# Kernel tuning notes

Hardware: AMD Instinct MI355X
Metric: run time of the kernel (lower is better)

The kernel has to match this reference:

```python
import jax, jax.numpy as jnp
import numpy as np

B, S, T, D = 4, 512, 512, 256


def setup_inputs() -> dict:
    key = jax.random.key(0)
    ks = jax.random.split(key, 10)
    scale = 1.0 / np.sqrt(D)
    return {
        "source": jax.random.normal(ks[0], (B, S, D), jnp.float32),
        "target": jax.random.normal(ks[1], (B, T, D), jnp.float32),
        "W_src": jax.random.uniform(ks[2], (D, D), jnp.float32, -scale, scale),
        "b_src": jax.random.uniform(ks[3], (D,), jnp.float32, -scale, scale),
        "W_tgt": jax.random.uniform(ks[4], (D, D), jnp.float32, -scale, scale),
        "b_tgt": jax.random.uniform(ks[5], (D,), jnp.float32, -scale, scale),
        "W_res": jax.random.uniform(ks[6], (D, 1), jnp.float32, -scale, scale),
        "b_res": jax.random.uniform(ks[7], (1,), jnp.float32, -scale, scale),
        "W_prob": jax.random.uniform(ks[8], (D, 2), jnp.float32, -scale, scale),
        "b_prob": jax.random.uniform(ks[9], (2,), jnp.float32, -scale, scale),
    }


def reference(source, target, W_src, b_src, W_tgt, b_tgt, W_res, b_res, W_prob, b_prob):
    # source: (B,S,D), target: (B,T,D)
    src_lin = jnp.einsum("bsd,de->bse", source, W_src) + b_src  # (B,S,D)
    tgt_lin = jnp.einsum("btd,de->bte", target, W_tgt) + b_tgt  # (B,T,D)
    # Bahdanau-style additive attention: (B,T,S,D) broadcast, tanh, D->1
    h = jnp.tanh(src_lin[:, None, :, :] + tgt_lin[:, :, None, :])  # (B,T,S,D)
    genP = jnp.einsum("btsd,d->bts", h, W_res[:, 0]) + b_res[0]     # (B,T,S)
    prob = jax.nn.softmax(jnp.einsum("btd,de->bte", target, W_prob) + b_prob, axis=-1)  # (B,T,2)
    return genP, prob
```

## Files before the change

kernel.cpp:

```cpp
#include <hip/hip_runtime.h>

#define B_ 4
#define S_ 512
#define T_ 512
#define D_ 256

#define K2F 2.8853900817779268f

__global__ __launch_bounds__(256) void lin_exp_kernel(
    const float* __restrict__ src, const float* __restrict__ tgt,
    const float* __restrict__ Wsrc, const float* __restrict__ bsrc,
    const float* __restrict__ Wtgt, const float* __restrict__ btgt,
    float* __restrict__ ya, float* __restrict__ yc)
{
    __shared__ float inT[D_ * 20];
    __shared__ float Wl[32 * D_];

    const int tid = threadIdx.x;
    const int nsrc_rows = B_ * S_;
    const int r0 = blockIdx.x * 16;
    const bool is_tgt = (r0 >= nsrc_rows);
    const float* in   = is_tgt ? tgt  : src;
    const float* W    = is_tgt ? Wtgt : Wsrc;
    const float* bias = is_tgt ? btgt : bsrc;
    float* out        = is_tgt ? yc   : ya;
    const int rbase   = is_tgt ? (r0 - nsrc_rows) : r0;

    {
        const int row = tid & 15;
        #pragma unroll
        for (int it = 0; it < 4; it++) {
            int kslot = it * 16 + (tid >> 4);
            int k4 = kslot * 4;
            float4 v = *(const float4*)&in[(rbase + row) * D_ + k4];
            inT[(k4 + 0) * 20 + row] = v.x;
            inT[(k4 + 1) * 20 + row] = v.y;
            inT[(k4 + 2) * 20 + row] = v.z;
            inT[(k4 + 3) * 20 + row] = v.w;
        }
    }

    const int rg = tid >> 6;
    const int cg = tid & 63;
    float acc[4][4];
    #pragma unroll
    for (int i = 0; i < 4; i++)
        #pragma unroll
        for (int j = 0; j < 4; j++) acc[i][j] = 0.f;

    for (int c0 = 0; c0 < D_; c0 += 32) {
        __syncthreads();
        #pragma unroll
        for (int it = 0; it < 8; it++) {
            int flat4 = it * 256 + tid;
            int wrow  = flat4 >> 6;
            int wcol4 = (flat4 & 63) * 4;
            *(float4*)&Wl[wrow * D_ + wcol4] =
                *(const float4*)&W[(c0 + wrow) * D_ + wcol4];
        }
        __syncthreads();
        #pragma unroll 8
        for (int kk = 0; kk < 32; kk++) {
            float4 av = *(const float4*)&inT[(c0 + kk) * 20 + 4 * rg];
            float4 wv = *(const float4*)&Wl[kk * D_ + 4 * cg];
            acc[0][0] = fmaf(av.x, wv.x, acc[0][0]);
            acc[0][1] = fmaf(av.x, wv.y, acc[0][1]);
            acc[0][2] = fmaf(av.x, wv.z, acc[0][2]);
            acc[0][3] = fmaf(av.x, wv.w, acc[0][3]);
            acc[1][0] = fmaf(av.y, wv.x, acc[1][0]);
            acc[1][1] = fmaf(av.y, wv.y, acc[1][1]);
            acc[1][2] = fmaf(av.y, wv.z, acc[1][2]);
            acc[1][3] = fmaf(av.y, wv.w, acc[1][3]);
            acc[2][0] = fmaf(av.z, wv.x, acc[2][0]);
            acc[2][1] = fmaf(av.z, wv.y, acc[2][1]);
            acc[2][2] = fmaf(av.z, wv.z, acc[2][2]);
            acc[2][3] = fmaf(av.z, wv.w, acc[2][3]);
            acc[3][0] = fmaf(av.w, wv.x, acc[3][0]);
            acc[3][1] = fmaf(av.w, wv.y, acc[3][1]);
            acc[3][2] = fmaf(av.w, wv.z, acc[3][2]);
            acc[3][3] = fmaf(av.w, wv.w, acc[3][3]);
        }
    }

    float4 bj = *(const float4*)&bias[4 * cg];
    #pragma unroll
    for (int i = 0; i < 4; i++) {
        float4 o;
        o.x = __builtin_amdgcn_exp2f((acc[i][0] + bj.x) * K2F);
        o.y = __builtin_amdgcn_exp2f((acc[i][1] + bj.y) * K2F);
        o.z = __builtin_amdgcn_exp2f((acc[i][2] + bj.z) * K2F);
        o.w = __builtin_amdgcn_exp2f((acc[i][3] + bj.w) * K2F);
        *(float4*)&out[(rbase + 4 * rg + i) * D_ + 4 * cg] = o;
    }
}

#define STR 68
__global__ __launch_bounds__(512) void genp_kernel(
    const float* __restrict__ ya, const float* __restrict__ yc,
    const float* __restrict__ Wres, const float* __restrict__ bres,
    float* __restrict__ out)
{
    __shared__ float la[64 * STR];
    __shared__ float lc[64 * STR];
    __shared__ float wl[D_];
    __shared__ float c0s;

    const int tid = threadIdx.x;
    const int s0 = blockIdx.x * 64;
    const int t0 = blockIdx.y * 64;
    const int b  = blockIdx.z;

    if (tid < D_) wl[tid] = Wres[tid];
    __syncthreads();
    if (tid == 0) {
        float s = bres[0];
        for (int d = 0; d < D_; d++) s += wl[d];
        c0s = s;
    }

    const float* abase = ya + (b * S_ + s0) * D_;
    const float* cbase = yc + (b * T_ + t0) * D_;

    const int m = tid & 15;
    const int g = tid >> 4;
    float acc[2][4] = {{0.f, 0.f, 0.f, 0.f}, {0.f, 0.f, 0.f, 0.f}};

    for (int d0 = 0; d0 < D_; d0 += 64) {
        __syncthreads();
        {
            const int k4  = (tid & 15) * 4;
            const int row = tid >> 4;
            #pragma unroll
            for (int it = 0; it < 2; it++) {
                int r = row + it * 32;
                float4 v = *(const float4*)&abase[r * D_ + d0 + k4];
                la[(k4 + 0) * STR + r] = v.x;
                la[(k4 + 1) * STR + r] = v.y;
                la[(k4 + 2) * STR + r] = v.z;
                la[(k4 + 3) * STR + r] = v.w;
                float4 u = *(const float4*)&cbase[r * D_ + d0 + k4];
                lc[(k4 + 0) * STR + r] = u.x;
                lc[(k4 + 1) * STR + r] = u.y;
                lc[(k4 + 2) * STR + r] = u.z;
                lc[(k4 + 3) * STR + r] = u.w;
            }
        }
        __syncthreads();
        #pragma unroll 4
        for (int k = 0; k < 64; k++) {
            float4 av = *(const float4*)&la[k * STR + 4 * m];
            float2 cv = *(const float2*)&lc[k * STR + 2 * g];
            float w = wl[d0 + k];
            float r00 = __builtin_amdgcn_rcpf(fmaf(cv.x, av.x, 1.f));
            float r01 = __builtin_amdgcn_rcpf(fmaf(cv.x, av.y, 1.f));
            float r02 = __builtin_amdgcn_rcpf(fmaf(cv.x, av.z, 1.f));
            float r03 = __builtin_amdgcn_rcpf(fmaf(cv.x, av.w, 1.f));
            float r10 = __builtin_amdgcn_rcpf(fmaf(cv.y, av.x, 1.f));
            float r11 = __builtin_amdgcn_rcpf(fmaf(cv.y, av.y, 1.f));
            float r12 = __builtin_amdgcn_rcpf(fmaf(cv.y, av.z, 1.f));
            float r13 = __builtin_amdgcn_rcpf(fmaf(cv.y, av.w, 1.f));
            acc[0][0] = fmaf(w, r00, acc[0][0]);
            acc[0][1] = fmaf(w, r01, acc[0][1]);
            acc[0][2] = fmaf(w, r02, acc[0][2]);
            acc[0][3] = fmaf(w, r03, acc[0][3]);
            acc[1][0] = fmaf(w, r10, acc[1][0]);
            acc[1][1] = fmaf(w, r11, acc[1][1]);
            acc[1][2] = fmaf(w, r12, acc[1][2]);
            acc[1][3] = fmaf(w, r13, acc[1][3]);
        }
    }

    const float C0 = c0s;
    #pragma unroll
    for (int i = 0; i < 2; i++) {
        int t = t0 + 2 * g + i;
        float4 o;
        o.x = C0 - 2.f * acc[i][0];
        o.y = C0 - 2.f * acc[i][1];
        o.z = C0 - 2.f * acc[i][2];
        o.w = C0 - 2.f * acc[i][3];
        *(float4*)&out[(b * T_ + t) * S_ + s0 + 4 * m] = o;
    }
}

__global__ __launch_bounds__(256) void prob_kernel(
    const float* __restrict__ tgt, const float* __restrict__ Wp,
    const float* __restrict__ bp, float* __restrict__ out)
{
    const int row  = blockIdx.x * 4 + (threadIdx.x >> 6);
    const int lane = threadIdx.x & 63;
    float p0 = 0.f, p1 = 0.f;
    #pragma unroll
    for (int i = 0; i < 4; i++) {
        int d = lane + i * 64;
        float v = tgt[row * D_ + d];
        float2 w = *(const float2*)&Wp[d * 2];
        p0 = fmaf(v, w.x, p0);
        p1 = fmaf(v, w.y, p1);
    }
    #pragma unroll
    for (int off = 32; off > 0; off >>= 1) {
        p0 += __shfl_down(p0, off, 64);
        p1 += __shfl_down(p1, off, 64);
    }
    if (lane == 0) {
        const float L2E = 1.4426950408889634f;
        float l0 = p0 + bp[0], l1 = p1 + bp[1];
        float e10 = __builtin_amdgcn_exp2f((l1 - l0) * L2E);
        float e01 = __builtin_amdgcn_exp2f((l0 - l1) * L2E);
        float q0 = __builtin_amdgcn_rcpf(1.f + e10);
        float q1 = __builtin_amdgcn_rcpf(1.f + e01);
        out[B_ * T_ * S_ + row * 2 + 0] = q0;
        out[B_ * T_ * S_ + row * 2 + 1] = q1;
    }
}

extern "C" void kernel_launch(void* const* d_in, const int* in_sizes, int n_in,
                              void* d_out, int out_size, void* d_ws, size_t ws_size,
                              hipStream_t stream) {
    const float* source = (const float*)d_in[0];
    const float* target = (const float*)d_in[1];
    const float* W_src  = (const float*)d_in[2];
    const float* b_src  = (const float*)d_in[3];
    const float* W_tgt  = (const float*)d_in[4];
    const float* b_tgt  = (const float*)d_in[5];
    const float* W_res  = (const float*)d_in[6];
    const float* b_res  = (const float*)d_in[7];
    const float* W_prob = (const float*)d_in[8];
    const float* b_prob = (const float*)d_in[9];
    float* out = (float*)d_out;

    float* ya = (float*)d_ws;
    float* yc = ya + B_ * S_ * D_;

    lin_exp_kernel<<<dim3((B_ * S_ + B_ * T_) / 16), 256, 0, stream>>>(
        source, target, W_src, b_src, W_tgt, b_tgt, ya, yc);
    genp_kernel<<<dim3(S_ / 64, T_ / 64, B_), 512, 0, stream>>>(
        ya, yc, W_res, b_res, out);
    prob_kernel<<<dim3(B_ * T_ / 4), 256, 0, stream>>>(
        target, W_prob, b_prob, out);
}
```

Measured before the change: 129.5 us.

## Use bf16 MFMA for projections and split genp over D with atomic accumulation

```diff
diff --git a/kernel.cpp b/kernel.cpp
--- a/kernel.cpp
+++ b/kernel.cpp
@@ -4,182 +4,175 @@
 #define S_ 512
 #define T_ 512
 #define D_ 256
-
+#define NSRC (B_ * S_)
 #define K2F 2.8853900817779268f
 
-__global__ __launch_bounds__(256) void lin_exp_kernel(
+typedef __attribute__((ext_vector_type(8))) short short8;
+typedef __attribute__((ext_vector_type(4))) float f32x4;
+
+__device__ __forceinline__ unsigned short f2bf(float f) {
+    union { float f; unsigned u; } v; v.f = f;
+    unsigned r = v.u + 0x7FFF + ((v.u >> 16) & 1);
+    return (unsigned short)(r >> 16);
+}
+
+__global__ __launch_bounds__(256) void cast_a_kernel(
     const float* __restrict__ src, const float* __restrict__ tgt,
-    const float* __restrict__ Wsrc, const float* __restrict__ bsrc,
-    const float* __restrict__ Wtgt, const float* __restrict__ btgt,
+    unsigned short* __restrict__ abf)
+{
+    int i4 = blockIdx.x * 256 + threadIdx.x;
+    const int half = NSRC * D_ / 4;
+    const float4* in = (i4 < half) ? (const float4*)src : (const float4*)tgt;
+    int j = (i4 < half) ? i4 : i4 - half;
+    float4 v = in[j];
+    ushort4 o;
+    o.x = f2bf(v.x); o.y = f2bf(v.y); o.z = f2bf(v.z); o.w = f2bf(v.w);
+    *(ushort4*)&abf[i4 * 4] = o;
+}
+
+__global__ __launch_bounds__(256) void cast_wt_kernel(
+    const float* __restrict__ Wsrc, const float* __restrict__ Wtgt,
+    unsigned short* __restrict__ wtb)
+{
+    int e = blockIdx.x >> 8;
+    int j = blockIdx.x & 255;
+    const float* W = e ? Wtgt : Wsrc;
+    int k = threadIdx.x;
+    wtb[(e * 256 + j) * D_ + k] = f2bf(W[k * D_ + j]);
+}
+
+__global__ __launch_bounds__(256) void lin_gemm_kernel(
+    const unsigned short* __restrict__ abf, const unsigned short* __restrict__ wtb,
+    const float* __restrict__ bsrc, const float* __restrict__ btgt,
     float* __restrict__ ya, float* __restrict__ yc)
 {
-    __shared__ float inT[D_ * 20];
-    __shared__ float Wl[32 * D_];
+    int wid  = blockIdx.x * 4 + (threadIdx.x >> 6);
+    int lane = threadIdx.x & 63;
+    int rg = wid >> 3;
+    int cg = wid & 7;
+    int e  = rg >> 7;
+    int r0 = rg * 16;
+    int n = lane & 15, quad = lane >> 4;
+
+    const float* bias = e ? btgt : bsrc;
+    float* out = e ? yc : ya;
+    int orow0 = r0 - e * NSRC;
+
+    int ct0 = cg * 2, ct1 = cg * 2 + 1;
+    f32x4 acc0 = {0.f, 0.f, 0.f, 0.f};
+    f32x4 acc1 = {0.f, 0.f, 0.f, 0.f};
+
+    const unsigned short* aP  = &abf[(r0 + n) * D_ + quad * 8];
+    const unsigned short* b0P = &wtb[(e * 256 + ct0 * 16 + n) * D_ + quad * 8];
+    const unsigned short* b1P = &wtb[(e * 256 + ct1 * 16 + n) * D_ + quad * 8];
+
+    #pragma unroll
+    for (int ks = 0; ks < 8; ks++) {
+        short8 a  = *(const short8*)&aP[ks * 32];
+        short8 b0 = *(const short8*)&b0P[ks * 32];
+        short8 b1 = *(const short8*)&b1P[ks * 32];
+        acc0 = __builtin_amdgcn_mfma_f32_16x16x32_bf16(a, b0, acc0, 0, 0, 0);
+        acc1 = __builtin_amdgcn_mfma_f32_16x16x32_bf16(a, b1, acc1, 0, 0, 0);
+    }
+
+    float b0v = bias[ct0 * 16 + n];
+    float b1v = bias[ct1 * 16 + n];
+    #pragma unroll
+    for (int i = 0; i < 4; i++) {
+        int row = orow0 + quad * 4 + i;
+        out[row * D_ + ct0 * 16 + n] = __builtin_amdgcn_exp2f((acc0[i] + b0v) * K2F);
+        out[row * D_ + ct1 * 16 + n] = __builtin_amdgcn_exp2f((acc1[i] + b1v) * K2F);
+    }
+}
+
+#define STR 68
+__global__ __launch_bounds__(256) void genp_kernel(
+    const float* __restrict__ ya, const float* __restrict__ yc,
+    const float* __restrict__ Wres, const float* __restrict__ bres,
+    float* __restrict__ out)
+{
+    __shared__ float la[64 * STR];
+    __shared__ float lc[64 * STR];
+    __shared__ float wl[64];
+    __shared__ float c0s;
 
     const int tid = threadIdx.x;
-    const int nsrc_rows = B_ * S_;
-    const int r0 = blockIdx.x * 16;
-    const bool is_tgt = (r0 >= nsrc_rows);
-    const float* in   = is_tgt ? tgt  : src;
-    const float* W    = is_tgt ? Wtgt : Wsrc;
-    const float* bias = is_tgt ? btgt : bsrc;
-    float* out        = is_tgt ? yc   : ya;
-    const int rbase   = is_tgt ? (r0 - nsrc_rows) : r0;
-
-    {
-        const int row = tid & 15;
+    const int w = tid >> 6, l = tid & 63;
+    const int s0 = blockIdx.x * 64;
+    const int t0 = blockIdx.y * 64;
+    const int b  = blockIdx.z >> 2;
+    const int dc = blockIdx.z & 3;
+    const int d0 = dc * 64;
+
+    const float* arow = &ya[(b * S_ + s0 + l) * D_ + d0];
+    const float* crow = &yc[(b * T_ + t0 + l) * D_ + d0];
+    #pragma unroll
+    for (int it = 0; it < 4; it++) {
+        int k4 = w * 16 + it * 4;
+        float4 va = *(const float4*)&arow[k4];
+        la[(k4 + 0) * STR + l] = va.x;
+        la[(k4 + 1) * STR + l] = va.y;
+        la[(k4 + 2) * STR + l] = va.z;
+        la[(k4 + 3) * STR + l] = va.w;
+        float4 vc = *(const float4*)&crow[k4];
+        lc[(k4 + 0) * STR + l] = vc.x;
+        lc[(k4 + 1) * STR + l] = vc.y;
+        lc[(k4 + 2) * STR + l] = vc.z;
+        lc[(k4 + 3) * STR + l] = vc.w;
+    }
+    if (tid < 64) wl[tid] = Wres[d0 + tid];
+    if (dc == 0 && w == 0) {
+        float s = Wres[l] + Wres[64 + l] + Wres[128 + l] + Wres[192 + l];
         #pragma unroll
-        for (int it = 0; it < 4; it++) {
-            int kslot = it * 16 + (tid >> 4);
-            int k4 = kslot * 4;
-            float4 v = *(const float4*)&in[(rbase + row) * D_ + k4];
-            inT[(k4 + 0) * 20 + row] = v.x;
-            inT[(k4 + 1) * 20 + row] = v.y;
-            inT[(k4 + 2) * 20 + row] = v.z;
-            inT[(k4 + 3) * 20 + row] = v.w;
-        }
-    }
-
-    const int rg = tid >> 6;
-    const int cg = tid & 63;
+        for (int off = 32; off > 0; off >>= 1) s += __shfl_down(s, off, 64);
+        if (l == 0) c0s = s + bres[0];
+    }
+    __syncthreads();
+
+    const int m = tid & 15;
+    const int g = tid >> 4;
     float acc[4][4];
     #pragma unroll
     for (int i = 0; i < 4; i++)
         #pragma unroll
         for (int j = 0; j < 4; j++) acc[i][j] = 0.f;
 
-    for (int c0 = 0; c0 < D_; c0 += 32) {
-        __syncthreads();
+    #pragma unroll 4
+    for (int k = 0; k < 64; k++) {
+        float4 av = *(const float4*)&la[k * STR + 4 * m];
+        float4 cv = *(const float4*)&lc[k * STR + 4 * g];
+        float wv = wl[k];
+        float a0 = av.x, a1 = av.y, a2 = av.z, a3 = av.w;
+        float c0 = cv.x, c1 = cv.y, c2 = cv.z, c3 = cv.w;
+        float r;
+        r = __builtin_amdgcn_rcpf(fmaf(c0, a0, 1.f)); acc[0][0] = fmaf(wv, r, acc[0][0]);
+        r = __builtin_amdgcn_rcpf(fmaf(c0, a1, 1.f)); acc[0][1] = fmaf(wv, r, acc[0][1]);
+        r = __builtin_amdgcn_rcpf(fmaf(c0, a2, 1.f)); acc[0][2] = fmaf(wv, r, acc[0][2]);
+        r = __builtin_amdgcn_rcpf(fmaf(c0, a3, 1.f)); acc[0][3] = fmaf(wv, r, acc[0][3]);
+        r = __builtin_amdgcn_rcpf(fmaf(c1, a0, 1.f)); acc[1][0] = fmaf(wv, r, acc[1][0]);
+        r = __builtin_amdgcn_rcpf(fmaf(c1, a1, 1.f)); acc[1][1] = fmaf(wv, r, acc[1][1]);
+        r = __builtin_amdgcn_rcpf(fmaf(c1, a2, 1.f)); acc[1][2] = fmaf(wv, r, acc[1][2]);
+        r = __builtin_amdgcn_rcpf(fmaf(c1, a3, 1.f)); acc[1][3] = fmaf(wv, r, acc[1][3]);
+        r = __builtin_amdgcn_rcpf(fmaf(c2, a0, 1.f)); acc[2][0] = fmaf(wv, r, acc[2][0]);
+        r = __builtin_amdgcn_rcpf(fmaf(c2, a1, 1.f)); acc[2][1] = fmaf(wv, r, acc[2][1]);
+        r = __builtin_amdgcn_rcpf(fmaf(c2, a2, 1.f)); acc[2][2] = fmaf(wv, r, acc[2][2]);
+        r = __builtin_amdgcn_rcpf(fmaf(c2, a3, 1.f)); acc[2][3] = fmaf(wv, r, acc[2][3]);
+        r = __builtin_amdgcn_rcpf(fmaf(c3, a0, 1.f)); acc[3][0] = fmaf(wv, r, acc[3][0]);
+        r = __builtin_amdgcn_rcpf(fmaf(c3, a1, 1.f)); acc[3][1] = fmaf(wv, r, acc[3][1]);
+        r = __builtin_amdgcn_rcpf(fmaf(c3, a2, 1.f)); acc[3][2] = fmaf(wv, r, acc[3][2]);
+        r = __builtin_amdgcn_rcpf(fmaf(c3, a3, 1.f)); acc[3][3] = fmaf(wv, r, acc[3][3]);
+    }
+
+    const float c0v = (dc == 0) ? c0s : 0.f;
+    #pragma unroll
+    for (int i = 0; i < 4; i++) {
+        int t = t0 + 4 * g + i;
+        float* o = &out[(b * T_ + t) * S_ + s0 + 4 * m];
         #pragma unroll
-        for (int it = 0; it < 8; it++) {
-            int flat4 = it * 256 + tid;
-            int wrow  = flat4 >> 6;
-            int wcol4 = (flat4 & 63) * 4;
-            *(float4*)&Wl[wrow * D_ + wcol4] =
-                *(const float4*)&W[(c0 + wrow) * D_ + wcol4];
+        for (int j = 0; j < 4; j++) {
+            __hip_atomic_fetch_add(&o[j], c0v - 2.f * acc[i][j],
+                                   __ATOMIC_RELAXED, __HIP_MEMORY_SCOPE_AGENT);
         }
-        __syncthreads();
-        #pragma unroll 8
-        for (int kk = 0; kk < 32; kk++) {
-            float4 av = *(const float4*)&inT[(c0 + kk) * 20 + 4 * rg];
-            float4 wv = *(const float4*)&Wl[kk * D_ + 4 * cg];
-            acc[0][0] = fmaf(av.x, wv.x, acc[0][0]);
-            acc[0][1] = fmaf(av.x, wv.y, acc[0][1]);
-            acc[0][2] = fmaf(av.x, wv.z, acc[0][2]);
-            acc[0][3] = fmaf(av.x, wv.w, acc[0][3]);
-            acc[1][0] = fmaf(av.y, wv.x, acc[1][0]);
-            acc[1][1] = fmaf(av.y, wv.y, acc[1][1]);
-            acc[1][2] = fmaf(av.y, wv.z, acc[1][2]);
-            acc[1][3] = fmaf(av.y, wv.w, acc[1][3]);
-            acc[2][0] = fmaf(av.z, wv.x, acc[2][0]);
-            acc[2][1] = fmaf(av.z, wv.y, acc[2][1]);
-            acc[2][2] = fmaf(av.z, wv.z, acc[2][2]);
-            acc[2][3] = fmaf(av.z, wv.w, acc[2][3]);
-            acc[3][0] = fmaf(av.w, wv.x, acc[3][0]);
-            acc[3][1] = fmaf(av.w, wv.y, acc[3][1]);
-            acc[3][2] = fmaf(av.w, wv.z, acc[3][2]);
-            acc[3][3] = fmaf(av.w, wv.w, acc[3][3]);
-        }
-    }
-
-    float4 bj = *(const float4*)&bias[4 * cg];
-    #pragma unroll
-    for (int i = 0; i < 4; i++) {
-        float4 o;
-        o.x = __builtin_amdgcn_exp2f((acc[i][0] + bj.x) * K2F);
-        o.y = __builtin_amdgcn_exp2f((acc[i][1] + bj.y) * K2F);
-        o.z = __builtin_amdgcn_exp2f((acc[i][2] + bj.z) * K2F);
-        o.w = __builtin_amdgcn_exp2f((acc[i][3] + bj.w) * K2F);
-        *(float4*)&out[(rbase + 4 * rg + i) * D_ + 4 * cg] = o;
-    }
-}
-
-#define STR 68
-__global__ __launch_bounds__(512) void genp_kernel(
-    const float* __restrict__ ya, const float* __restrict__ yc,
-    const float* __restrict__ Wres, const float* __restrict__ bres,
-    float* __restrict__ out)
-{
-    __shared__ float la[64 * STR];
-    __shared__ float lc[64 * STR];
-    __shared__ float wl[D_];
-    __shared__ float c0s;
-
-    const int tid = threadIdx.x;
-    const int s0 = blockIdx.x * 64;
-    const int t0 = blockIdx.y * 64;
-    const int b  = blockIdx.z;
-
-    if (tid < D_) wl[tid] = Wres[tid];
-    __syncthreads();
-    if (tid == 0) {
-        float s = bres[0];
-        for (int d = 0; d < D_; d++) s += wl[d];
-        c0s = s;
-    }
-
-    const float* abase = ya + (b * S_ + s0) * D_;
-    const float* cbase = yc + (b * T_ + t0) * D_;
-
-    const int m = tid & 15;
-    const int g = tid >> 4;
-    float acc[2][4] = {{0.f, 0.f, 0.f, 0.f}, {0.f, 0.f, 0.f, 0.f}};
-
-    for (int d0 = 0; d0 < D_; d0 += 64) {
-        __syncthreads();
-        {
-            const int k4  = (tid & 15) * 4;
-            const int row = tid >> 4;
-            #pragma unroll
-            for (int it = 0; it < 2; it++) {
-                int r = row + it * 32;
-                float4 v = *(const float4*)&abase[r * D_ + d0 + k4];
-                la[(k4 + 0) * STR + r] = v.x;
-                la[(k4 + 1) * STR + r] = v.y;
-                la[(k4 + 2) * STR + r] = v.z;
-                la[(k4 + 3) * STR + r] = v.w;
-                float4 u = *(const float4*)&cbase[r * D_ + d0 + k4];
-                lc[(k4 + 0) * STR + r] = u.x;
-                lc[(k4 + 1) * STR + r] = u.y;
-                lc[(k4 + 2) * STR + r] = u.z;
-                lc[(k4 + 3) * STR + r] = u.w;
-            }
-        }
-        __syncthreads();
-        #pragma unroll 4
-        for (int k = 0; k < 64; k++) {
-            float4 av = *(const float4*)&la[k * STR + 4 * m];
-            float2 cv = *(const float2*)&lc[k * STR + 2 * g];
-            float w = wl[d0 + k];
-            float r00 = __builtin_amdgcn_rcpf(fmaf(cv.x, av.x, 1.f));
-            float r01 = __builtin_amdgcn_rcpf(fmaf(cv.x, av.y, 1.f));
-            float r02 = __builtin_amdgcn_rcpf(fmaf(cv.x, av.z, 1.f));
-            float r03 = __builtin_amdgcn_rcpf(fmaf(cv.x, av.w, 1.f));
-            float r10 = __builtin_amdgcn_rcpf(fmaf(cv.y, av.x, 1.f));
-            float r11 = __builtin_amdgcn_rcpf(fmaf(cv.y, av.y, 1.f));
-            float r12 = __builtin_amdgcn_rcpf(fmaf(cv.y, av.z, 1.f));
-            float r13 = __builtin_amdgcn_rcpf(fmaf(cv.y, av.w, 1.f));
-            acc[0][0] = fmaf(w, r00, acc[0][0]);
-            acc[0][1] = fmaf(w, r01, acc[0][1]);
-            acc[0][2] = fmaf(w, r02, acc[0][2]);
-            acc[0][3] = fmaf(w, r03, acc[0][3]);
-            acc[1][0] = fmaf(w, r10, acc[1][0]);
-            acc[1][1] = fmaf(w, r11, acc[1][1]);
-            acc[1][2] = fmaf(w, r12, acc[1][2]);
-            acc[1][3] = fmaf(w, r13, acc[1][3]);
-        }
-    }
-
-    const float C0 = c0s;
-    #pragma unroll
-    for (int i = 0; i < 2; i++) {
-        int t = t0 + 2 * g + i;
-        float4 o;
-        o.x = C0 - 2.f * acc[i][0];
-        o.y = C0 - 2.f * acc[i][1];
-        o.z = C0 - 2.f * acc[i][2];
-        o.w = C0 - 2.f * acc[i][3];
-        *(float4*)&out[(b * T_ + t) * S_ + s0 + 4 * m] = o;
     }
 }
 
@@ -208,10 +201,8 @@
         float l0 = p0 + bp[0], l1 = p1 + bp[1];
         float e10 = __builtin_amdgcn_exp2f((l1 - l0) * L2E);
         float e01 = __builtin_amdgcn_exp2f((l0 - l1) * L2E);
-        float q0 = __builtin_amdgcn_rcpf(1.f + e10);
-        float q1 = __builtin_amdgcn_rcpf(1.f + e01);
-        out[B_ * T_ * S_ + row * 2 + 0] = q0;
-        out[B_ * T_ * S_ + row * 2 + 1] = q1;
+        out[B_ * T_ * S_ + row * 2 + 0] = __builtin_amdgcn_rcpf(1.f + e10);
+        out[B_ * T_ * S_ + row * 2 + 1] = __builtin_amdgcn_rcpf(1.f + e01);
     }
 }
 
@@ -231,12 +222,15 @@
     float* out = (float*)d_out;
 
     float* ya = (float*)d_ws;
-    float* yc = ya + B_ * S_ * D_;
-
-    lin_exp_kernel<<<dim3((B_ * S_ + B_ * T_) / 16), 256, 0, stream>>>(
-        source, target, W_src, b_src, W_tgt, b_tgt, ya, yc);
-    genp_kernel<<<dim3(S_ / 64, T_ / 64, B_), 512, 0, stream>>>(
-        ya, yc, W_res, b_res, out);
-    prob_kernel<<<dim3(B_ * T_ / 4), 256, 0, stream>>>(
-        target, W_prob, b_prob, out);
-}
+    float* yc = ya + NSRC * D_;
+    unsigned short* abf = (unsigned short*)(yc + NSRC * D_);
+    unsigned short* wtb = abf + 2 * NSRC * D_;
+
+    hipMemsetAsync(out, 0, (size_t)(B_ * T_ * S_) * sizeof(float), stream);
+
+    cast_a_kernel<<<1024, 256, 0, stream>>>(source, target, abf);
+    cast_wt_kernel<<<512, 256, 0, stream>>>(W_src, W_tgt, wtb);
+    lin_gemm_kernel<<<512, 256, 0, stream>>>(abf, wtb, b_src, b_tgt, ya, yc);
+    genp_kernel<<<dim3(8, 8, 16), 256, 0, stream>>>(ya, yc, W_res, b_res, out);
+    prob_kernel<<<B_ * T_ / 4, 256, 0, stream>>>(target, W_prob, b_prob, out);
+}
```

New measurement: 163.0 us. +25.9%, slower.
